# Kernel optimization log

Measured on AMD Instinct MI355X. Metric: run time of the kernel, lower is better.

The kernel has to match this reference:

```python
import jax, jax.numpy as jnp
import numpy as np


def _filters():
    ident = jnp.array([[0., 0., 0.], [0., 1., 0.], [0., 0., 0.]], jnp.float32)
    sobel_x = jnp.array([[-1., 0., 1.], [-2., 0., 2.], [-1., 0., 1.]], jnp.float32)
    lap = jnp.array([[1., 2., 1.], [2., -12., 2.], [1., 2., 1.]], jnp.float32)
    return jnp.stack([ident, sobel_x, sobel_x.T, lap])  # [4,3,3]


def _perception(x):
    # depthwise conv with 4 fixed filters, circular padding; matches torch
    # reshape(b*ch,1,h,w) -> conv -> reshape(b, ch*4, h, w) channel ordering
    b, c, h, w = x.shape
    xp = jnp.pad(x, ((0, 0), (0, 0), (1, 1), (1, 1)), mode='wrap')
    y = xp.reshape(b * c, 1, h + 2, w + 2)
    k = _filters()[:, None]  # [4,1,3,3]
    y = jax.lax.conv_general_dilated(
        y, k, window_strides=(1, 1), padding='VALID',
        dimension_numbers=('NCHW', 'OIHW', 'NCHW'))  # [b*c,4,h,w]
    return y.reshape(b, c * 4, h, w)


def setup_inputs() -> dict:
    key = jax.random.key(0)
    k1, k2, k3, k4, k5 = jax.random.split(key, 5)
    B, C, H, W = 32, 12, 256, 256
    FC = 96
    xavier_std = 0.2 * np.sqrt(2.0 / (4 * C + FC))  # xavier_normal gain=0.2
    return {
        'x': jax.random.normal(k1, (B, C, H, W), jnp.float32),
        'w1': jax.random.normal(k2, (FC, 4 * C), jnp.float32) * xavier_std,
        'b1': jax.random.normal(k3, (FC,), jnp.float32) * 0.01,
        'w2': jax.random.normal(k4, (C, FC), jnp.float32) * 0.02,
        'rand_mask': jax.random.uniform(k5, (B, 1, H, W), jnp.float32),
    }


def reference(x, w1, b1, w2, rand_mask):
    update_rate = 0.5
    y = _perception(x)  # [B, 4C, H, W]
    hidden = jax.nn.relu(jnp.einsum('oc,bchw->bohw', w1, y) + b1[None, :, None, None])
    y = jnp.einsum('oc,bchw->bohw', w2, hidden)  # [B, C, H, W]
    update_mask = jnp.floor(rand_mask + update_rate)  # bernoulli(update_rate)
    return x + y * update_mask
```

## Files before the change

### kernel.cpp

```cpp
#include <hip/hip_runtime.h>
#include <stdint.h>

#define NC 12
#define NHW (256*256)
#define RSTR 72
#define CSTR 432

typedef __attribute__((ext_vector_type(8))) short bf16x8;
typedef __attribute__((ext_vector_type(4))) float f32x4;
typedef __attribute__((ext_vector_type(4))) uint32_t u32x4;
typedef __attribute__((ext_vector_type(2))) __bf16 bf16x2v;

__device__ __forceinline__ uint32_t pkbf(float lo, float hi) {
    uint32_t r;
    asm("v_cvt_pk_bf16_f32 %0, %1, %2" : "=v"(r) : "v"(lo), "v"(hi));
    return r;
}
__device__ __forceinline__ uint32_t pkbf_c(float lo, float hi) {
    bf16x2v v = { (__bf16)lo, (__bf16)hi };
    return __builtin_bit_cast(uint32_t, v);
}
#define PIN(v) asm volatile("" : "+v"(v))

__global__ __launch_bounds__(256, 4) void nca_fused10(
    const float* __restrict__ x, const float* __restrict__ w1,
    const float* __restrict__ b1, const float* __restrict__ w2,
    const float* __restrict__ rmask, float* __restrict__ out)
{
    __shared__ float smem[12 * CSTR];

    const int tid  = threadIdx.x;
    const int lane = tid & 63;
    const int wv   = tid >> 6;
    const int g    = lane >> 4;
    const int p    = lane & 15;
    const int c0   = 3 * g;

    u32x4 a1u[6][2];
    f32x4 biasv[6];
    #pragma unroll
    for (int t = 0; t < 6; ++t) {
        const int row = 16*t + p;
        const float4 fa = *reinterpret_cast<const float4*>(w1 + row*48 + 12*g + 0);
        const float4 fb = *reinterpret_cast<const float4*>(w1 + row*48 + 12*g + 4);
        const float4 fc = *reinterpret_cast<const float4*>(w1 + row*48 + 12*g + 8);
        a1u[t][0] = (u32x4){ pkbf_c(fa.x, fa.y), pkbf_c(fa.z, fa.w), pkbf_c(fb.x, fb.y), pkbf_c(fb.z, fb.w) };
        a1u[t][1] = (u32x4){ pkbf_c(fc.x, fc.y), pkbf_c(fc.z, fc.w), 0u, 0u };
        biasv[t] = *reinterpret_cast<const f32x4*>(b1 + 16*t + 4*g);
        PIN(a1u[t][0]); PIN(a1u[t][1]); PIN(biasv[t]);
    }
    u32x4 a2u[3];
    {
        const int rp = p & 3, gp = p >> 2;
        const int chA = 3*gp + rp;
        #pragma unroll
        for (int s = 0; s < 3; ++s) {
            u32x4 u = {0u, 0u, 0u, 0u};
            if (rp < 3) {
                const float4 wa = *reinterpret_cast<const float4*>(w2 + chA*96 + 32*s + 4*g);
                const float4 wb = *reinterpret_cast<const float4*>(w2 + chA*96 + 32*s + 16 + 4*g);
                u = (u32x4){ pkbf_c(wa.x, wa.y), pkbf_c(wa.z, wa.w), pkbf_c(wb.x, wb.y), pkbf_c(wb.z, wb.w) };
            }
            a2u[s] = u;
            PIN(a2u[s]);
        }
    }

    const int b    = blockIdx.x >> 8;
    const int rem  = blockIdx.x & 255;
    const int ra   = (rem >> 2) << 2;
    const int c0q  = (rem & 3) << 6;
    const float* __restrict__ xb = x + (size_t)b * NC * NHW;
    const float* __restrict__ mb = rmask + (size_t)b * NHW;
    float* __restrict__ ob = out + (size_t)b * NC * NHW;

    {
        #pragma unroll
        for (int k = 0; k < 5; ++k) {
            const int u = tid + (k << 8);
            if (k < 4 || tid < 128) {
                const int pair  = u >> 4;
                const int chunk = u & 15;
                const int c  = pair / 6;
                const int r_ = pair - 6*c;
                const int row = (ra + 255 + r_) & 255;
                const f32x4 v = *reinterpret_cast<const f32x4*>(xb + c*NHW + (row << 8) + c0q + (chunk << 2));
                *reinterpret_cast<f32x4*>(&smem[c*CSTR + r_*RSTR + 4 + (chunk << 2)]) = v;
            }
        }
        if (tid < 144) {
            const int hr  = tid >> 1;
            const int side= tid & 1;
            const int c   = hr / 6;
            const int r_  = hr - 6*c;
            const int row = (ra + 255 + r_) & 255;
            const int col = side ? ((c0q + 64) & 255) : ((c0q + 255) & 255);
            smem[c*CSTR + r_*RSTR + (side ? 68 : 3)] = xb[c*NHW + (row << 8) + col];
        }
    }
    __syncthreads();

    const int h    = ra + wv;
    const int hrow = h << 8;

    int tb[3];
    #pragma unroll
    for (int ci = 0; ci < 3; ++ci) tb[ci] = (c0 + ci)*CSTR + wv*RSTR + 3 + p;
    float* obp[3];
    #pragma unroll
    for (int r = 0; r < 3; ++r) obp[r] = ob + (c0 + r)*NHW + hrow + c0q + p;
    const float* mbp = mb + hrow + c0q + p;

    #pragma unroll
    for (int grp = 0; grp < 4; ++grp) {
        const int o = grp << 4;

        uint32_t yw[6];
        float xm[3];
        #pragma unroll
        for (int ci = 0; ci < 3; ++ci) {
            const int tbc = tb[ci] + o;
            const float v0 = smem[tbc+0],        v1 = smem[tbc+1],        v2 = smem[tbc+2];
            const float v3 = smem[tbc+RSTR],     v4 = smem[tbc+RSTR+1],   v5 = smem[tbc+RSTR+2];
            const float v6 = smem[tbc+2*RSTR],   v7 = smem[tbc+2*RSTR+1], v8 = smem[tbc+2*RSTR+2];
            const float s0 = v0 + v2, d0 = v2 - v0;
            const float s1 = v3 + v5, d1 = v5 - v3;
            const float s2 = v6 + v8, d2 = v8 - v6;
            const float t0 = fmaf(2.f, v1, s0);
            const float t2 = fmaf(2.f, v7, s2);
            const float fsx = fmaf(2.f, d1, d0 + d2);
            const float fsy = t2 - t0;
            const float lap = fmaf(-12.f, v4, fmaf(2.f, s1, t0 + t2));
            yw[2*ci]   = pkbf(v4, fsx);
            yw[2*ci+1] = pkbf(fsy, lap);
            xm[ci] = v4;
        }
        const bf16x8 yf0 = __builtin_bit_cast(bf16x8, (u32x4){yw[0], yw[1], yw[2], yw[3]});
        const bf16x8 yf1 = __builtin_bit_cast(bf16x8, (u32x4){yw[4], yw[5], 0u, 0u});

        __builtin_amdgcn_s_setprio(1);
        uint32_t pu[6][2];
        #pragma unroll
        for (int t = 0; t < 6; ++t) {
            f32x4 acc = biasv[t];
            acc = __builtin_amdgcn_mfma_f32_16x16x32_bf16(__builtin_bit_cast(bf16x8, a1u[t][0]), yf0, acc, 0, 0, 0);
            acc = __builtin_amdgcn_mfma_f32_16x16x32_bf16(__builtin_bit_cast(bf16x8, a1u[t][1]), yf1, acc, 0, 0, 0);
            pu[t][0] = pkbf(fmaxf(acc[0], 0.f), fmaxf(acc[1], 0.f));
            pu[t][1] = pkbf(fmaxf(acc[2], 0.f), fmaxf(acc[3], 0.f));
        }
        f32x4 acc2 = {0.f, 0.f, 0.f, 0.f};
        #pragma unroll
        for (int s2 = 0; s2 < 3; ++s2) {
            const u32x4 fb2 = { pu[2*s2][0], pu[2*s2][1], pu[2*s2+1][0], pu[2*s2+1][1] };
            acc2 = __builtin_amdgcn_mfma_f32_16x16x32_bf16(__builtin_bit_cast(bf16x8, a2u[s2]), __builtin_bit_cast(bf16x8, fb2), acc2, 0, 0, 0);
        }
        __builtin_amdgcn_s_setprio(0);

        const float um = floorf(mbp[o] + 0.5f);
        #pragma unroll
        for (int r = 0; r < 3; ++r)
            obp[r][o] = xm[r] + acc2[r] * um;
    }
}

extern "C" void kernel_launch(void* const* d_in, const int* in_sizes, int n_in,
                              void* d_out, int out_size, void* d_ws, size_t ws_size,
                              hipStream_t stream) {
    const float* x  = (const float*)d_in[0];
    const float* w1 = (const float*)d_in[1];
    const float* b1 = (const float*)d_in[2];
    const float* w2 = (const float*)d_in[3];
    const float* rm = (const float*)d_in[4];
    float* out = (float*)d_out;
    nca_fused10<<<dim3(32 * 64 * 4), dim3(256), 0, stream>>>(x, w1, b1, w2, rm, out);
}
```

Measured before the change: 92.66 us.

## Widen tiles to 128 columns, fold bias into MFMA, pin weights in AGPRs

Each block now covers a 4-row by 128-column strip instead of 64 columns, which halves the block count and reduces halo/overlap reloads per output. The bias is folded into the first-layer MFMA by placing it in a spare K slot of the weight fragment and a constant 1.0 in the matching input slot, freeing the bias registers. Weight fragments are pinned to accumulation registers (AGPRs) instead of VGPRs to relieve VGPR pressure. LDS use doubles to about 39KB per block, which may limit occupancy, and the bias is now rounded to bf16.

Result: slower. 104.3 us (+12.6%).

```diff
diff --git a/kernel.cpp b/kernel.cpp
--- a/kernel.cpp
+++ b/kernel.cpp
@@ -3,8 +3,8 @@
 
 #define NC 12
 #define NHW (256*256)
-#define RSTR 72
-#define CSTR 432
+#define RSTR 136
+#define CSTR 816
 
 typedef __attribute__((ext_vector_type(8))) short bf16x8;
 typedef __attribute__((ext_vector_type(4))) float f32x4;
@@ -20,9 +20,9 @@
     bf16x2v v = { (__bf16)lo, (__bf16)hi };
     return __builtin_bit_cast(uint32_t, v);
 }
-#define PIN(v) asm volatile("" : "+v"(v))
+#define PINA(v) asm volatile("" : "+a"(v))
 
-__global__ __launch_bounds__(256, 4) void nca_fused10(
+__global__ __launch_bounds__(256, 4) void nca_fused11(
     const float* __restrict__ x, const float* __restrict__ w1,
     const float* __restrict__ b1, const float* __restrict__ w2,
     const float* __restrict__ rmask, float* __restrict__ out)
@@ -37,17 +37,16 @@
     const int c0   = 3 * g;
 
     u32x4 a1u[6][2];
-    f32x4 biasv[6];
     #pragma unroll
     for (int t = 0; t < 6; ++t) {
         const int row = 16*t + p;
         const float4 fa = *reinterpret_cast<const float4*>(w1 + row*48 + 12*g + 0);
         const float4 fb = *reinterpret_cast<const float4*>(w1 + row*48 + 12*g + 4);
         const float4 fc = *reinterpret_cast<const float4*>(w1 + row*48 + 12*g + 8);
+        const uint32_t biasw = (g == 0) ? pkbf_c(b1[row], 0.f) : 0u;
         a1u[t][0] = (u32x4){ pkbf_c(fa.x, fa.y), pkbf_c(fa.z, fa.w), pkbf_c(fb.x, fb.y), pkbf_c(fb.z, fb.w) };
-        a1u[t][1] = (u32x4){ pkbf_c(fc.x, fc.y), pkbf_c(fc.z, fc.w), 0u, 0u };
-        biasv[t] = *reinterpret_cast<const f32x4*>(b1 + 16*t + 4*g);
-        PIN(a1u[t][0]); PIN(a1u[t][1]); PIN(biasv[t]);
+        a1u[t][1] = (u32x4){ pkbf_c(fc.x, fc.y), pkbf_c(fc.z, fc.w), biasw, 0u };
+        PINA(a1u[t][0]); PINA(a1u[t][1]);
     }
     u32x4 a2u[3];
     {
@@ -62,31 +61,31 @@
                 u = (u32x4){ pkbf_c(wa.x, wa.y), pkbf_c(wa.z, wa.w), pkbf_c(wb.x, wb.y), pkbf_c(wb.z, wb.w) };
             }
             a2u[s] = u;
-            PIN(a2u[s]);
+            PINA(a2u[s]);
         }
     }
+    const uint32_t one_c = (g == 0) ? 0x00003F80u : 0u;
 
-    const int b    = blockIdx.x >> 8;
-    const int rem  = blockIdx.x & 255;
-    const int ra   = (rem >> 2) << 2;
-    const int c0q  = (rem & 3) << 6;
+    const int b     = blockIdx.x >> 7;
+    const int strip = (blockIdx.x >> 1) & 63;
+    const int half  = blockIdx.x & 1;
+    const int ra    = strip << 2;
+    const int c0g   = half << 7;
     const float* __restrict__ xb = x + (size_t)b * NC * NHW;
     const float* __restrict__ mb = rmask + (size_t)b * NHW;
     float* __restrict__ ob = out + (size_t)b * NC * NHW;
 
     {
+        const int q = tid >> 5;
+        const int l = tid & 31;
         #pragma unroll
-        for (int k = 0; k < 5; ++k) {
-            const int u = tid + (k << 8);
-            if (k < 4 || tid < 128) {
-                const int pair  = u >> 4;
-                const int chunk = u & 15;
-                const int c  = pair / 6;
-                const int r_ = pair - 6*c;
-                const int row = (ra + 255 + r_) & 255;
-                const f32x4 v = *reinterpret_cast<const f32x4*>(xb + c*NHW + (row << 8) + c0q + (chunk << 2));
-                *reinterpret_cast<f32x4*>(&smem[c*CSTR + r_*RSTR + 4 + (chunk << 2)]) = v;
-            }
+        for (int j = 0; j < 9; ++j) {
+            const int hr  = 8*j + q;
+            const int c   = hr / 6;
+            const int r_  = hr - 6*c;
+            const int row = (ra + 255 + r_) & 255;
+            const f32x4 v = *reinterpret_cast<const f32x4*>(xb + c*NHW + (row << 8) + c0g + (l << 2));
+            *reinterpret_cast<f32x4*>(&smem[c*CSTR + r_*RSTR + 4 + (l << 2)]) = v;
         }
         if (tid < 144) {
             const int hr  = tid >> 1;
@@ -94,8 +93,8 @@
             const int c   = hr / 6;
             const int r_  = hr - 6*c;
             const int row = (ra + 255 + r_) & 255;
-            const int col = side ? ((c0q + 64) & 255) : ((c0q + 255) & 255);
-            smem[c*CSTR + r_*RSTR + (side ? 68 : 3)] = xb[c*NHW + (row << 8) + col];
+            const int col = side ? ((c0g + 128) & 255) : ((c0g + 255) & 255);
+            smem[c*CSTR + r_*RSTR + (side ? 132 : 3)] = xb[c*NHW + (row << 8) + col];
         }
     }
     __syncthreads();
@@ -108,11 +107,11 @@
     for (int ci = 0; ci < 3; ++ci) tb[ci] = (c0 + ci)*CSTR + wv*RSTR + 3 + p;
     float* obp[3];
     #pragma unroll
-    for (int r = 0; r < 3; ++r) obp[r] = ob + (c0 + r)*NHW + hrow + c0q + p;
-    const float* mbp = mb + hrow + c0q + p;
+    for (int r = 0; r < 3; ++r) obp[r] = ob + (c0 + r)*NHW + hrow + c0g + p;
+    const float* mbp = mb + hrow + c0g + p;
 
     #pragma unroll
-    for (int grp = 0; grp < 4; ++grp) {
+    for (int grp = 0; grp < 8; ++grp) {
         const int o = grp << 4;
 
         uint32_t yw[6];
@@ -136,13 +135,13 @@
             xm[ci] = v4;
         }
         const bf16x8 yf0 = __builtin_bit_cast(bf16x8, (u32x4){yw[0], yw[1], yw[2], yw[3]});
-        const bf16x8 yf1 = __builtin_bit_cast(bf16x8, (u32x4){yw[4], yw[5], 0u, 0u});
+        const bf16x8 yf1 = __builtin_bit_cast(bf16x8, (u32x4){yw[4], yw[5], one_c, 0u});
 
         __builtin_amdgcn_s_setprio(1);
         uint32_t pu[6][2];
         #pragma unroll
         for (int t = 0; t < 6; ++t) {
-            f32x4 acc = biasv[t];
+            f32x4 acc = {0.f, 0.f, 0.f, 0.f};
             acc = __builtin_amdgcn_mfma_f32_16x16x32_bf16(__builtin_bit_cast(bf16x8, a1u[t][0]), yf0, acc, 0, 0, 0);
             acc = __builtin_amdgcn_mfma_f32_16x16x32_bf16(__builtin_bit_cast(bf16x8, a1u[t][1]), yf1, acc, 0, 0, 0);
             pu[t][0] = pkbf(fmaxf(acc[0], 0.f), fmaxf(acc[1], 0.f));
@@ -172,5 +171,5 @@
     const float* w2 = (const float*)d_in[3];
     const float* rm = (const float*)d_in[4];
     float* out = (float*)d_out;
-    nca_fused10<<<dim3(32 * 64 * 4), dim3(256), 0, stream>>>(x, w1, b1, w2, rm, out);
+    nca_fused11<<<dim3(32 * 64 * 2), dim3(256), 0, stream>>>(x, w1, b1, w2, rm, out);
 }
```
